# Kernel tuning notes

Measured on AMD Instinct MI355X. Metric: run time of the kernel, lower is better.

The kernel has to match this reference:

```python
import jax, jax.numpy as jnp
import numpy as np

# Architecture constants (from init_kwargs)
A, L, NCF = 200, 10, 9            # num_agent, in_len, num_control_features
D_MODEL, N_HEADS = 1024, 4
HEAD_DIM = D_MODEL // N_HEADS      # 256 (the module's 'head_dim')
PER_HEAD = HEAD_DIM // N_HEADS     # 64 (effective per-head dim after rearrange)
SCALE = HEAD_DIM ** -0.5           # module scales by head_dim**-0.5
N = A * L + NCF                    # 2009 tokens


def _build_mask():
    # block-diagonal agent mask: eye(A) repeat_interleaved L on both axes,
    # then zero-padded by NCF rows/cols for control features
    m = np.kron(np.eye(A, dtype=np.float32), np.ones((L, L), dtype=np.float32))
    m = np.pad(m, ((0, NCF), (0, NCF)))
    return jnp.asarray(m)  # [N, N]

_MASK = _build_mask()


def setup_inputs() -> dict:
    key = jax.random.key(0)
    k0, k1, k2, k3 = jax.random.split(key, 4)
    x = jax.random.normal(k0, (4, N, D_MODEL), jnp.float32)
    W_qkv = jax.random.normal(k1, (D_MODEL, HEAD_DIM * 3), jnp.float32) * 0.02
    W_qk_self = jax.random.normal(k2, (D_MODEL, HEAD_DIM * 2), jnp.float32) * 0.02
    W_out = jax.random.normal(k3, (HEAD_DIM, D_MODEL), jnp.float32) * 0.02
    b_out = jnp.zeros((D_MODEL,), jnp.float32)
    return {"x": x, "W_qkv": W_qkv, "W_qk_self": W_qk_self,
            "W_out": W_out, "b_out": b_out}


def _heads(t, b, n):
    # 'b n (h d) -> b h n d' with h = N_HEADS
    return t.reshape(b, n, N_HEADS, PER_HEAD).transpose(0, 2, 1, 3)


def reference(x, W_qkv, W_qk_self, W_out, b_out):
    b, n, _ = x.shape
    q, k, v = jnp.split(x @ W_qkv, 3, axis=-1)          # each [b, n, HEAD_DIM]
    q, k, v = _heads(q, b, n), _heads(k, b, n), _heads(v, b, n)  # [b,h,n,d]
    q_self, k_self = jnp.split(x @ W_qk_self, 2, axis=-1)
    q_self, k_self = _heads(q_self, b, n), _heads(k_self, b, n)

    dots = jnp.einsum('bhnd,bhmd->bhnm', q, k) * SCALE
    dots_self = jnp.einsum('bhnd,bhmd->bhnm', q_self, k_self) * SCALE
    dots_all = _MASK * dots_self + (1.0 - _MASK) * dots  # blend via block mask
    attn = jax.nn.softmax(dots_all, axis=-1)             # [b,h,n,n]

    out = jnp.einsum('bhnm,bhmd->bhnd', attn, v)
    out = out.transpose(0, 2, 1, 3).reshape(b, n, HEAD_DIM)  # 'b h n d -> b n (h d)'
    out = out @ W_out + b_out                            # to_out (dropout=0)
    return out, attn
```

## Files before the change

### kernel.cpp

```cpp
#include <hip/hip_runtime.h>

typedef unsigned short u16;
typedef unsigned int u32;
typedef short short8 __attribute__((ext_vector_type(8)));
typedef float f32x4 __attribute__((ext_vector_type(4)));
typedef float f32x16 __attribute__((ext_vector_type(16)));

#define NTOK 2009
#define M8   8036
#define DMOD 1024
#define PKBH 129024

static __device__ __forceinline__ u16 f2bf(float f) {
  unsigned int x = __float_as_uint(f);
  x += 0x7fffu + ((x >> 16) & 1u);
  return (u16)(x >> 16);
}
static __device__ __forceinline__ float bf2f(u16 u) {
  return __uint_as_float((unsigned int)u << 16);
}
static __device__ __forceinline__ u32 pk2(float a, float b) {
  return (u32)f2bf(a) | ((u32)f2bf(b) << 16);
}
static __device__ __forceinline__ u32 cvtpk(float a, float b) {
  u32 d;
  asm("v_cvt_pk_bf16_f32 %0, %1, %2" : "=v"(d) : "v"(a), "v"(b));
  return d;
}
static __device__ __forceinline__ void gload_lds16(const void* g, void* l) {
  __builtin_amdgcn_global_load_lds(
      (const __attribute__((address_space(1))) void*)g,
      (__attribute__((address_space(3))) void*)l, 16, 0, 0);
}

__global__ void k_conv_x(const float* __restrict__ x, u16* __restrict__ xb) {
  int i = blockIdx.x * 256 + threadIdx.x;
  float4 v = ((const float4*)x)[i];
  unsigned int a = (unsigned int)f2bf(v.x) | ((unsigned int)f2bf(v.y) << 16);
  unsigned int b = (unsigned int)f2bf(v.z) | ((unsigned int)f2bf(v.w) << 16);
  ((uint2*)xb)[i] = make_uint2(a, b);
}

__global__ void k_conv_wcat(const float* __restrict__ Wqkv, const float* __restrict__ Wqs,
                            u16* __restrict__ WtCat) {
  int i = blockIdx.x * 256 + threadIdx.x;
  int n = i >> 10, k = i & 1023;
  float v = (n < 768) ? Wqkv[k * 768 + n] : Wqs[k * 512 + (n - 768)];
  WtCat[i] = f2bf(v);
}

__global__ void k_conv_wout(const float* __restrict__ Wout, u16* __restrict__ WtOut) {
  int i = blockIdx.x * 256 + threadIdx.x;
  int n = i >> 8, k = i & 255;
  WtOut[i] = f2bf(Wout[k * 1024 + n]);
}

__global__ __launch_bounds__(256) void k_gemm_proj(
    const u16* __restrict__ A, const u16* __restrict__ Bt,
    u16* __restrict__ Qp, u16* __restrict__ Kp, u16* __restrict__ Vp,
    u16* __restrict__ Qsb, u16* __restrict__ Ksb)
{
  __shared__ u16 Asm[128 * 64];
  __shared__ u16 Bsm[128 * 64];
  int mt = blockIdx.x * 128, nt = blockIdx.y * 128;
  int tid = threadIdx.x, lane = tid & 63, w = tid >> 6;
  int wm = w >> 1, wn = w & 1;
  int fr = lane & 15, fq = lane >> 4;
  int srow = w * 32 + (lane >> 3);
  int scol = (lane & 7) * 8;
  f32x4 acc[4][4];
#pragma unroll
  for (int a = 0; a < 4; ++a)
#pragma unroll
    for (int b = 0; b < 4; ++b) acc[a][b] = (f32x4){0.f, 0.f, 0.f, 0.f};

  for (int kt = 0; kt < 1024; kt += 64) {
#pragma unroll
    for (int j = 0; j < 4; ++j) {
      int r = srow + j * 8;
      int am = mt + r; if (am >= M8) am = 0;
      gload_lds16(A + (size_t)am * 1024 + kt + scol, Asm + (size_t)(w * 32 + j * 8) * 64);
      gload_lds16(Bt + (size_t)(nt + r) * 1024 + kt + scol, Bsm + (size_t)(w * 32 + j * 8) * 64);
    }
    __syncthreads();
#pragma unroll
    for (int cs = 0; cs < 2; ++cs) {
      short8 af[4], bf[4];
#pragma unroll
      for (int i = 0; i < 4; ++i) {
        af[i] = *(const short8*)&Asm[(size_t)(wm * 64 + i * 16 + fr) * 64 + cs * 32 + fq * 8];
        bf[i] = *(const short8*)&Bsm[(size_t)(wn * 64 + i * 16 + fr) * 64 + cs * 32 + fq * 8];
      }
#pragma unroll
      for (int mi = 0; mi < 4; ++mi)
#pragma unroll
        for (int ni = 0; ni < 4; ++ni)
          acc[mi][ni] = __builtin_amdgcn_mfma_f32_16x16x32_bf16(af[mi], bf[ni], acc[mi][ni], 0, 0, 0);
    }
    __syncthreads();
  }

#pragma unroll
  for (int ni = 0; ni < 4; ++ni) {
    int n = nt + wn * 64 + ni * 16 + fr;
    int g = n >> 6, d = n & 63;
    int h = g & 3, sel = g >> 2;
    float scl = (sel == 0 || sel == 3) ? 0.0625f : 1.0f;
#pragma unroll
    for (int mi = 0; mi < 4; ++mi) {
#pragma unroll
      for (int i = 0; i < 4; ++i) {
        int m = mt + wm * 64 + mi * 16 + fq * 4 + i;
        if (m >= M8) continue;
        int b_ = m / NTOK, tok = m - b_ * NTOK;
        int bh = b_ * 4 + h;
        u16 val = f2bf(acc[mi][ni][i] * scl);
        if (sel <= 1) {
          u16* dst = sel == 0 ? Qp : Kp;
          size_t idx = ((((size_t)bh * 63 + (tok >> 5)) * 4 + (d >> 4)) * 2 + ((d >> 3) & 1)) * 256
                       + (tok & 31) * 8 + (d & 7);
          dst[idx] = val;
        } else if (sel == 2) {
          size_t idx = (((((size_t)bh * 63 + (tok >> 5)) * 2 + (d >> 5)) * 2 + ((tok >> 4) & 1)) * 2
                        + ((tok >> 3) & 1)) * 256 + (d & 31) * 8 + (tok & 7);
          Vp[idx] = val;
        } else {
          u16* p = (sel == 3) ? Qsb : Ksb;
          p[((size_t)bh * NTOK + tok) * 64 + d] = val;
        }
      }
    }
  }
}

__global__ void k_self(const u16* __restrict__ Qs, const u16* __restrict__ Ks,
                       float* __restrict__ selfS) {
  int blk = blockIdx.x;
  int bh = blk / 200, a = blk % 200;
  int t = threadIdx.x;
  if (t >= 100) return;
  int ri = t / 10, rj = t % 10;
  const u16* qp = &Qs[((size_t)bh * NTOK + a * 10 + ri) * 64];
  const u16* kp = &Ks[((size_t)bh * NTOK + a * 10 + rj) * 64];
  float s = 0.f;
#pragma unroll 8
  for (int k = 0; k < 64; ++k) s += bf2f(qp[k]) * bf2f(kp[k]);
  selfS[(size_t)blk * 100 + t] = s;
}

__global__ __launch_bounds__(256, 2) void k_attn10(
    const u16* __restrict__ Qp, const u16* __restrict__ Kp,
    const u16* __restrict__ Vp, const float* __restrict__ selfS,
    float* __restrict__ attn, u16* __restrict__ Ob)
{
  __shared__ float s_sum[4][32];
  __shared__ float s_inv[32];
  __shared__ float s_o[4][64][32];
  int bh = blockIdx.x;
  int qt = blockIdx.y;
  int q0 = qt * 32;
  int tid = threadIdx.x;
  int lane = tid & 63, w = tid >> 6;
  int ql = lane & 31, h = lane >> 5;
  int qg = q0 + ql;
  int lo8 = ql * 8;

  const u16* qbase = Qp + (size_t)bh * PKBH + (size_t)qt * 2048;
  const u16* kbase = Kp + (size_t)bh * PKBH;
  const u16* vbase = Vp + (size_t)bh * PKBH;

  short8 qf[4];
#pragma unroll
  for (int c = 0; c < 4; ++c)
    qf[c] = *(const short8*)&qbase[(c * 2 + h) * 256 + lo8];

  int qa = (qg < 2000) ? (qg / 10) : -1;
  int band_lo = 1 << 30, band_hi = -(1 << 30);
  if (q0 < 2000) {
    int hi_row = (q0 + 31 < 1999) ? q0 + 31 : 1999;
    band_lo = (q0 / 10) * 10;
    band_hi = (hi_row / 10) * 10 + 10;
  }
  const float* sfb = &selfS[(size_t)bh * 20000];

  int t0 = w * 16;
  int t1 = t0 + 16; if (t1 > 63) t1 = 63;

  u32 pb[16][8];
  short8 kf[4], kfn[4], vf[4];
  f32x16 oacc0 = {}, oacc1 = {};

#pragma unroll
  for (int c = 0; c < 4; ++c)
    kf[c] = *(const short8*)&kbase[(size_t)t0 * 2048 + (c * 2 + h) * 256 + lo8];
  float ssum = 0.f;
#pragma unroll
  for (int i = 0; i < 16; ++i) {
    int t = t0 + i;
    if (t < t1) {
      int tn = (t + 1 < t1) ? t + 1 : t0;
#pragma unroll
      for (int c = 0; c < 4; ++c)
        vf[c] = *(const short8*)&vbase[(size_t)t * 2048 + (c * 2 + h) * 256 + lo8];
#pragma unroll
      for (int c = 0; c < 4; ++c)
        kfn[c] = *(const short8*)&kbase[(size_t)tn * 2048 + (c * 2 + h) * 256 + lo8];
      f32x16 acc = {};
#pragma unroll
      for (int c = 0; c < 4; ++c)
        acc = __builtin_amdgcn_mfma_f32_32x32x16_bf16(kf[c], qf[c], acc, 0, 0, 0);
      int kt = t * 32;
      float e[16];
      if ((kt < band_hi) && (kt + 32 > band_lo)) {
#pragma unroll
        for (int r = 0; r < 16; ++r) {
          int kc = kt + (r & 3) + 8 * (r >> 2) + 4 * h;
          float sc = acc[r];
          if (qa >= 0 && kc < 2000 && (kc / 10) == qa)
            sc = sfb[qa * 100 + (qg - qa * 10) * 10 + (kc - qa * 10)];
          e[r] = __expf(sc);
        }
      } else {
#pragma unroll
        for (int r = 0; r < 16; ++r) e[r] = __expf(acc[r]);
      }
      if (t == 62) {
#pragma unroll
        for (int r = 0; r < 16; ++r) {
          int kc = kt + (r & 3) + 8 * (r >> 2) + 4 * h;
          if (kc >= NTOK) e[r] = 0.f;
        }
      }
#pragma unroll
      for (int r2 = 0; r2 < 8; ++r2) {
        pb[i][r2] = cvtpk(e[2 * r2], e[2 * r2 + 1]);
        ssum += e[2 * r2] + e[2 * r2 + 1];
      }
      u32 p00 = __shfl_xor(pb[i][0], 32), p01 = __shfl_xor(pb[i][1], 32);
      u32 p10 = __shfl_xor(pb[i][2], 32), p11 = __shfl_xor(pb[i][3], 32);
      u32 p20 = __shfl_xor(pb[i][4], 32), p21 = __shfl_xor(pb[i][5], 32);
      u32 p30 = __shfl_xor(pb[i][6], 32), p31 = __shfl_xor(pb[i][7], 32);
      u32 b0[4], b1[4];
      b0[0] = h ? p10 : pb[i][0];  b0[1] = h ? p11 : pb[i][1];
      b0[2] = h ? pb[i][2] : p00;  b0[3] = h ? pb[i][3] : p01;
      b1[0] = h ? p30 : pb[i][4];  b1[1] = h ? p31 : pb[i][5];
      b1[2] = h ? pb[i][6] : p20;  b1[3] = h ? pb[i][7] : p21;
      short8 B0, B1;
      __builtin_memcpy(&B0, b0, 16);
      __builtin_memcpy(&B1, b1, 16);
      oacc0 = __builtin_amdgcn_mfma_f32_32x32x16_bf16(vf[0], B0, oacc0, 0, 0, 0);
      oacc1 = __builtin_amdgcn_mfma_f32_32x32x16_bf16(vf[2], B0, oacc1, 0, 0, 0);
      oacc0 = __builtin_amdgcn_mfma_f32_32x32x16_bf16(vf[1], B1, oacc0, 0, 0, 0);
      oacc1 = __builtin_amdgcn_mfma_f32_32x32x16_bf16(vf[3], B1, oacc1, 0, 0, 0);
#pragma unroll
      for (int c = 0; c < 4; ++c) kf[c] = kfn[c];
    }
  }
  ssum += __shfl_xor(ssum, 32);
  if (lane < 32) s_sum[w][ql] = ssum;
  __syncthreads();
  if (tid < 32)
    s_inv[tid] = 1.0f / (s_sum[0][tid] + s_sum[1][tid] + s_sum[2][tid] + s_sum[3][tid]);
  __syncthreads();

  u32* stage = (u32*)&s_o[w][0][0];
  int kwbase = t0 * 32;
#pragma unroll
  for (int cs = 0; cs < 4; ++cs) {
#pragma unroll
    for (int i2 = 0; i2 < 4; ++i2) {
      int t = t0 + cs * 4 + i2;
      if (t < t1) {
#pragma unroll
        for (int r2 = 0; r2 < 8; ++r2) {
          int c = i2 * 16 + ((r2 & 1) + 4 * (r2 >> 1) + 2 * h);
          stage[ql * 64 + (c ^ (ql & 31))] = pb[cs * 4 + i2][r2];
        }
      }
    }
#pragma unroll
    for (int s = 0; s < 64; ++s) {
      int R = s >> 1, hf = s & 1;
      int grow = q0 + R;
      if (grow < NTOK) {
        int col = kwbase + cs * 128 + hf * 64 + lane;
        if (col < NTOK) {
          u32 u = stage[R * 64 + ((hf * 32 + (lane >> 1)) ^ (R & 31))];
          float f = __uint_as_float((lane & 1) ? (u & 0xffff0000u) : (u << 16)) * s_inv[R];
          attn[((size_t)bh * NTOK + grow) * NTOK + col] = f;
        }
      }
    }
  }
  __syncthreads();

#pragma unroll
  for (int r = 0; r < 16; ++r) {
    int d = (r & 3) + 8 * (r >> 2) + 4 * h;
    s_o[w][d][ql] = oacc0[r];
    s_o[w][d + 32][ql] = oacc1[r];
  }
  __syncthreads();
  {
    int q = tid & 31, dg = tid >> 5;
    int qg2 = q0 + q;
    if (qg2 < NTOK) {
      float invq = s_inv[q];
      int b_ = bh >> 2, hd = bh & 3;
      u16* orow = &Ob[((size_t)(b_ * NTOK + qg2)) * 256 + hd * 64 + dg * 8];
      u32 wpk[4];
#pragma unroll
      for (int j = 0; j < 4; ++j) {
        int d = dg * 8 + 2 * j;
        float a = (s_o[0][d][q] + s_o[1][d][q] + s_o[2][d][q] + s_o[3][d][q]) * invq;
        float b = (s_o[0][d + 1][q] + s_o[1][d + 1][q] + s_o[2][d + 1][q] + s_o[3][d + 1][q]) * invq;
        wpk[j] = pk2(a, b);
      }
      *(uint4*)orow = make_uint4(wpk[0], wpk[1], wpk[2], wpk[3]);
    }
  }
}

__global__ __launch_bounds__(256) void k_gemm_out(
    const u16* __restrict__ A, const u16* __restrict__ Bt,
    const float* __restrict__ bias, float* __restrict__ C)
{
  __shared__ u16 Asm[128 * 64];
  __shared__ u16 Bsm[128 * 64];
  int mt = blockIdx.x * 128, nt = blockIdx.y * 128;
  int tid = threadIdx.x, lane = tid & 63, w = tid >> 6;
  int wm = w >> 1, wn = w & 1;
  int fr = lane & 15, fq = lane >> 4;
  int srow = w * 32 + (lane >> 3);
  int scol = (lane & 7) * 8;
  f32x4 acc[4][4];
#pragma unroll
  for (int a = 0; a < 4; ++a)
#pragma unroll
    for (int b = 0; b < 4; ++b) acc[a][b] = (f32x4){0.f, 0.f, 0.f, 0.f};

  for (int kt = 0; kt < 256; kt += 64) {
#pragma unroll
    for (int j = 0; j < 4; ++j) {
      int r = srow + j * 8;
      int am = mt + r; if (am >= M8) am = 0;
      gload_lds16(A + (size_t)am * 256 + kt + scol, Asm + (size_t)(w * 32 + j * 8) * 64);
      gload_lds16(Bt + (size_t)(nt + r) * 256 + kt + scol, Bsm + (size_t)(w * 32 + j * 8) * 64);
    }
    __syncthreads();
#pragma unroll
    for (int cs = 0; cs < 2; ++cs) {
      short8 af[4], bf[4];
#pragma unroll
      for (int i = 0; i < 4; ++i) {
        af[i] = *(const short8*)&Asm[(size_t)(wm * 64 + i * 16 + fr) * 64 + cs * 32 + fq * 8];
        bf[i] = *(const short8*)&Bsm[(size_t)(wn * 64 + i * 16 + fr) * 64 + cs * 32 + fq * 8];
      }
#pragma unroll
      for (int mi = 0; mi < 4; ++mi)
#pragma unroll
        for (int ni = 0; ni < 4; ++ni)
          acc[mi][ni] = __builtin_amdgcn_mfma_f32_16x16x32_bf16(af[mi], bf[ni], acc[mi][ni], 0, 0, 0);
    }
    __syncthreads();
  }

#pragma unroll
  for (int ni = 0; ni < 4; ++ni) {
    int n = nt + wn * 64 + ni * 16 + fr;
    float bn = bias[n];
#pragma unroll
    for (int mi = 0; mi < 4; ++mi)
#pragma unroll
      for (int i = 0; i < 4; ++i) {
        int m = mt + wm * 64 + mi * 16 + fq * 4 + i;
        if (m < M8) C[(size_t)m * DMOD + n] = acc[mi][ni][i] + bn;
      }
  }
}

extern "C" void kernel_launch(void* const* d_in, const int* in_sizes, int n_in,
                              void* d_out, int out_size, void* d_ws, size_t ws_size,
                              hipStream_t stream) {
  (void)in_sizes; (void)n_in; (void)out_size; (void)ws_size;
  const float* x    = (const float*)d_in[0];
  const float* Wqkv = (const float*)d_in[1];
  const float* Wqs  = (const float*)d_in[2];
  const float* Wout = (const float*)d_in[3];
  const float* bout = (const float*)d_in[4];
  float* out  = (float*)d_out;
  float* attn = out + (size_t)M8 * DMOD;

  char* ws = (char*)d_ws;
  u16*   xb    = (u16*)(ws);
  u16*   WtCat = (u16*)(ws + 16457728);
  u16*   WtOut = (u16*)(ws + 19079168);
  u16*   Qp    = (u16*)(ws + 19603456);
  u16*   Kp    = (u16*)(ws + 23732224);
  u16*   Vp    = (u16*)(ws + 27860992);
  u16*   Qsb   = (u16*)(ws + 31989760);
  u16*   Ksb   = (u16*)(ws + 36104192);
  u16*   Ob    = (u16*)(ws + 40218624);
  float* selfS = (float*)(ws + 44333056);

  k_conv_x<<<dim3(8036), dim3(256), 0, stream>>>(x, xb);
  k_conv_wcat<<<dim3(5120), dim3(256), 0, stream>>>(Wqkv, Wqs, WtCat);
  k_conv_wout<<<dim3(1024), dim3(256), 0, stream>>>(Wout, WtOut);
  k_gemm_proj<<<dim3(63, 10), dim3(256), 0, stream>>>(xb, WtCat, Qp, Kp, Vp, Qsb, Ksb);
  k_self<<<dim3(3200), dim3(128), 0, stream>>>(Qsb, Ksb, selfS);
  k_attn10<<<dim3(16, 63), dim3(256), 0, stream>>>(Qp, Kp, Vp, selfS, attn, Ob);
  k_gemm_out<<<dim3(63, 8), dim3(256), 0, stream>>>(Ob, WtOut, bout, out);
}
```

Baseline: 216.0 us.

## Split attention key range across 16 waves and merge conversion kernels

The attention kernel moves from 256 to 1024 threads per block. Each of the 16 waves now handles 4 key tiles instead of 16, which cuts per-thread register use for the stored probabilities and raises parallelism. Per-wave partial outputs are reduced in two stages through LDS, and the attn write loop is reshaped for 64-column chunks. The three fp32-to-bf16 conversion kernels are merged into one launch to save launch overhead. The cost is more block-wide synchronisation and more LDS reduction work per block.

```diff
diff --git a/kernel.cpp b/kernel.cpp
--- a/kernel.cpp
+++ b/kernel.cpp
@@ -33,26 +33,27 @@
       (__attribute__((address_space(3))) void*)l, 16, 0, 0);
 }
 
-__global__ void k_conv_x(const float* __restrict__ x, u16* __restrict__ xb) {
-  int i = blockIdx.x * 256 + threadIdx.x;
-  float4 v = ((const float4*)x)[i];
-  unsigned int a = (unsigned int)f2bf(v.x) | ((unsigned int)f2bf(v.y) << 16);
-  unsigned int b = (unsigned int)f2bf(v.z) | ((unsigned int)f2bf(v.w) << 16);
-  ((uint2*)xb)[i] = make_uint2(a, b);
-}
-
-__global__ void k_conv_wcat(const float* __restrict__ Wqkv, const float* __restrict__ Wqs,
-                            u16* __restrict__ WtCat) {
-  int i = blockIdx.x * 256 + threadIdx.x;
-  int n = i >> 10, k = i & 1023;
-  float v = (n < 768) ? Wqkv[k * 768 + n] : Wqs[k * 512 + (n - 768)];
-  WtCat[i] = f2bf(v);
-}
-
-__global__ void k_conv_wout(const float* __restrict__ Wout, u16* __restrict__ WtOut) {
-  int i = blockIdx.x * 256 + threadIdx.x;
-  int n = i >> 8, k = i & 255;
-  WtOut[i] = f2bf(Wout[k * 1024 + n]);
+__global__ void k_convs(const float* __restrict__ x, u16* __restrict__ xb,
+                        const float* __restrict__ Wqkv, const float* __restrict__ Wqs,
+                        u16* __restrict__ WtCat,
+                        const float* __restrict__ Wout, u16* __restrict__ WtOut) {
+  int blk = blockIdx.x;
+  if (blk < 8036) {
+    int i = blk * 256 + threadIdx.x;
+    float4 v = ((const float4*)x)[i];
+    unsigned int a = (unsigned int)f2bf(v.x) | ((unsigned int)f2bf(v.y) << 16);
+    unsigned int b = (unsigned int)f2bf(v.z) | ((unsigned int)f2bf(v.w) << 16);
+    ((uint2*)xb)[i] = make_uint2(a, b);
+  } else if (blk < 8036 + 5120) {
+    int i = (blk - 8036) * 256 + threadIdx.x;
+    int n = i >> 10, k = i & 1023;
+    float v = (n < 768) ? Wqkv[k * 768 + n] : Wqs[k * 512 + (n - 768)];
+    WtCat[i] = f2bf(v);
+  } else {
+    int i = (blk - 8036 - 5120) * 256 + threadIdx.x;
+    int n = i >> 8, k = i & 255;
+    WtOut[i] = f2bf(Wout[k * 1024 + n]);
+  }
 }
 
 __global__ __launch_bounds__(256) void k_gemm_proj(
@@ -148,14 +149,14 @@
   selfS[(size_t)blk * 100 + t] = s;
 }
 
-__global__ __launch_bounds__(256, 2) void k_attn10(
+__global__ __launch_bounds__(1024, 4) void k_attn11(
     const u16* __restrict__ Qp, const u16* __restrict__ Kp,
     const u16* __restrict__ Vp, const float* __restrict__ selfS,
     float* __restrict__ attn, u16* __restrict__ Ob)
 {
-  __shared__ float s_sum[4][32];
+  __shared__ float s_sum[16][32];
   __shared__ float s_inv[32];
-  __shared__ float s_o[4][64][32];
+  __shared__ float s_o[8][64][32];
   int bh = blockIdx.x;
   int qt = blockIdx.y;
   int q0 = qt * 32;
@@ -183,10 +184,10 @@
   }
   const float* sfb = &selfS[(size_t)bh * 20000];
 
-  int t0 = w * 16;
-  int t1 = t0 + 16; if (t1 > 63) t1 = 63;
-
-  u32 pb[16][8];
+  int t0 = w * 4;
+  int t1 = t0 + 4; if (t1 > 63) t1 = 63;
+
+  u32 pb[4][8];
   short8 kf[4], kfn[4], vf[4];
   f32x16 oacc0 = {}, oacc1 = {};
 
@@ -195,7 +196,7 @@
     kf[c] = *(const short8*)&kbase[(size_t)t0 * 2048 + (c * 2 + h) * 256 + lo8];
   float ssum = 0.f;
 #pragma unroll
-  for (int i = 0; i < 16; ++i) {
+  for (int i = 0; i < 4; ++i) {
     int t = t0 + i;
     if (t < t1) {
       int tn = (t + 1 < t1) ? t + 1 : t0;
@@ -259,64 +260,71 @@
   ssum += __shfl_xor(ssum, 32);
   if (lane < 32) s_sum[w][ql] = ssum;
   __syncthreads();
-  if (tid < 32)
-    s_inv[tid] = 1.0f / (s_sum[0][tid] + s_sum[1][tid] + s_sum[2][tid] + s_sum[3][tid]);
+  if (tid < 32) {
+    float tot = 0.f;
+#pragma unroll
+    for (int s = 0; s < 16; ++s) tot += s_sum[s][tid];
+    s_inv[tid] = 1.0f / tot;
+  }
   __syncthreads();
 
-  u32* stage = (u32*)&s_o[w][0][0];
-  int kwbase = t0 * 32;
-#pragma unroll
-  for (int cs = 0; cs < 4; ++cs) {
-#pragma unroll
-    for (int i2 = 0; i2 < 4; ++i2) {
-      int t = t0 + cs * 4 + i2;
+  u32* stage = (u32*)(((char*)s_o) + w * 4096);
+#pragma unroll
+  for (int cs = 0; cs < 2; ++cs) {
+#pragma unroll
+    for (int i2 = 0; i2 < 2; ++i2) {
+      int t = t0 + cs * 2 + i2;
       if (t < t1) {
 #pragma unroll
         for (int r2 = 0; r2 < 8; ++r2) {
           int c = i2 * 16 + ((r2 & 1) + 4 * (r2 >> 1) + 2 * h);
-          stage[ql * 64 + (c ^ (ql & 31))] = pb[cs * 4 + i2][r2];
+          stage[ql * 32 + (c ^ (ql & 31))] = pb[cs * 2 + i2][r2];
         }
       }
     }
 #pragma unroll
-    for (int s = 0; s < 64; ++s) {
-      int R = s >> 1, hf = s & 1;
+    for (int R = 0; R < 32; ++R) {
       int grow = q0 + R;
-      if (grow < NTOK) {
-        int col = kwbase + cs * 128 + hf * 64 + lane;
-        if (col < NTOK) {
-          u32 u = stage[R * 64 + ((hf * 32 + (lane >> 1)) ^ (R & 31))];
-          float f = __uint_as_float((lane & 1) ? (u & 0xffff0000u) : (u << 16)) * s_inv[R];
-          attn[((size_t)bh * NTOK + grow) * NTOK + col] = f;
-        }
+      int col = t0 * 32 + cs * 64 + lane;
+      if (grow < NTOK && col < NTOK) {
+        u32 u = stage[R * 32 + (((lane >> 1)) ^ (R & 31))];
+        float f = __uint_as_float((lane & 1) ? (u & 0xffff0000u) : (u << 16)) * s_inv[R];
+        attn[((size_t)bh * NTOK + grow) * NTOK + col] = f;
       }
     }
   }
   __syncthreads();
 
-#pragma unroll
-  for (int r = 0; r < 16; ++r) {
-    int d = (r & 3) + 8 * (r >> 2) + 4 * h;
-    s_o[w][d][ql] = oacc0[r];
-    s_o[w][d + 32][ql] = oacc1[r];
+  if (w >= 8) {
+#pragma unroll
+    for (int r = 0; r < 16; ++r) {
+      int d = (r & 3) + 8 * (r >> 2) + 4 * h;
+      s_o[w - 8][d][ql] = oacc0[r];
+      s_o[w - 8][d + 32][ql] = oacc1[r];
+    }
+  }
+  __syncthreads();
+  if (w < 8) {
+#pragma unroll
+    for (int r = 0; r < 16; ++r) {
+      int d = (r & 3) + 8 * (r >> 2) + 4 * h;
+      s_o[w][d][ql] += oacc0[r];
+      s_o[w][d + 32][ql] += oacc1[r];
+    }
   }
   __syncthreads();
   {
-    int q = tid & 31, dg = tid >> 5;
+    int q = tid & 31, dp = tid >> 5;
     int qg2 = q0 + q;
     if (qg2 < NTOK) {
       float invq = s_inv[q];
+      int d = dp * 2;
+      float a = 0.f, b = 0.f;
+#pragma unroll
+      for (int s = 0; s < 8; ++s) { a += s_o[s][d][q]; b += s_o[s][d + 1][q]; }
       int b_ = bh >> 2, hd = bh & 3;
-      u16* orow = &Ob[((size_t)(b_ * NTOK + qg2)) * 256 + hd * 64 + dg * 8];
-      u32 wpk[4];
-#pragma unroll
-      for (int j = 0; j < 4; ++j) {
-        int d = dg * 8 + 2 * j;
-        float a = (s_o[0][d][q] + s_o[1][d][q] + s_o[2][d][q] + s_o[3][d][q]) * invq;
-        float b = (s_o[0][d + 1][q] + s_o[1][d + 1][q] + s_o[2][d + 1][q] + s_o[3][d + 1][q]) * invq;
-        wpk[j] = pk2(a, b);
-      }
-      *(uint4*)orow = make_uint4(wpk[0], wpk[1], wpk[2], wpk[3]);
+      u32* orow = (u32*)&Ob[((size_t)(b_ * NTOK + qg2)) * 256 + hd * 64];
+      orow[dp] = pk2(a * invq, b * invq);
     }
   }
 }
@@ -403,11 +411,10 @@
   u16*   Ob    = (u16*)(ws + 40218624);
   float* selfS = (float*)(ws + 44333056);
 
-  k_conv_x<<<dim3(8036), dim3(256), 0, stream>>>(x, xb);
-  k_conv_wcat<<<dim3(5120), dim3(256), 0, stream>>>(Wqkv, Wqs, WtCat);
-  k_conv_wout<<<dim3(1024), dim3(256), 0, stream>>>(Wout, WtOut);
+  k_convs<<<dim3(8036 + 5120 + 1024), dim3(256), 0, stream>>>(
+      x, xb, Wqkv, Wqs, WtCat, Wout, WtOut);
   k_gemm_proj<<<dim3(63, 10), dim3(256), 0, stream>>>(xb, WtCat, Qp, Kp, Vp, Qsb, Ksb);
   k_self<<<dim3(3200), dim3(128), 0, stream>>>(Qsb, Ksb, selfS);
-  k_attn10<<<dim3(16, 63), dim3(256), 0, stream>>>(Qp, Kp, Vp, selfS, attn, Ob);
+  k_attn11<<<dim3(16, 63), dim3(1024), 0, stream>>>(Qp, Kp, Vp, selfS, attn, Ob);
   k_gemm_out<<<dim3(63, 8), dim3(256), 0, stream>>>(Ob, WtOut, bout, out);
 }
```

After: 248.0 us. +14.8%, slower.
